# Performance work log

Hardware: AMD Instinct MI355X
Metric: run time of the kernel (lower is better)

Reference implementation:

```python
import jax, jax.numpy as jnp
import numpy as np

N_NODES = 100000


def _gcn_layer(h, W, b, src, dst, norm, n):
    # h: [N, Fin] -> transform then normalized scatter-add aggregation
    h = h @ W                                   # [N, Fout]
    msg = h[src] * norm[:, None]                # [E', Fout] gather + scale
    out = jax.ops.segment_sum(msg, dst, num_segments=n)  # scatter-add
    return out + b


def setup_inputs() -> dict:
    key = jax.random.key(0)
    k1, k2, k3, k4 = jax.random.split(key, 4)
    N, F_IN, HID, C, E = N_NODES, 512, 128, 40, 1600000
    x = jax.random.normal(k1, (N, F_IN), dtype=jnp.float32)
    edge_index = jax.random.randint(k2, (2, E), 0, N, dtype=jnp.int64)
    W1 = jax.random.normal(k3, (F_IN, HID), dtype=jnp.float32) * (1.0 / np.sqrt(F_IN))
    b1 = jnp.zeros((HID,), dtype=jnp.float32)
    W2 = jax.random.normal(k4, (HID, C), dtype=jnp.float32) * (1.0 / np.sqrt(HID))
    b2 = jnp.zeros((C,), dtype=jnp.float32)
    return {"x": x, "edge_index": edge_index, "W1": W1, "b1": b1, "W2": W2, "b2": b2}


def reference(x, edge_index, W1, b1, W2, b2):
    n = x.shape[0]
    # add self-loops (GCNConv default)
    loop = jnp.arange(n, dtype=edge_index.dtype)
    src = jnp.concatenate([edge_index[0], loop])
    dst = jnp.concatenate([edge_index[1], loop])
    # symmetric normalization: deg counted on destination (in-degree, incl. self-loop)
    deg = jax.ops.segment_sum(jnp.ones_like(dst, dtype=x.dtype), dst, num_segments=n)
    dis = jnp.where(deg > 0, jax.lax.rsqrt(deg), 0.0)  # deg^{-1/2}
    norm = dis[src] * dis[dst]                          # per-edge weight

    h = jax.nn.relu(_gcn_layer(x, W1, b1, src, dst, norm, n))
    # dropout: identity in eval mode (training=False)
    h = _gcn_layer(h, W2, b2, src, dst, norm, n)
    return jax.nn.log_softmax(h, axis=1)
```

## Files before the change

kernel.cpp:

```cpp
#include <hip/hip_runtime.h>
#include <hip/hip_bf16.h>


#define F_IN 512
#define HID  128
#define NC   40

typedef __attribute__((ext_vector_type(8))) short bf16x8;
typedef __attribute__((ext_vector_type(4))) float f32x4v;

__device__ __forceinline__ ushort f2bf(float f) {
    union { float f; unsigned u; } x; x.f = f;
    unsigned r = x.u + 0x7FFFu + ((x.u >> 16) & 1u);
    return (ushort)(r >> 16);
}
__device__ __forceinline__ float bf2f(ushort u) {
    return __uint_as_float((unsigned)u << 16);
}

__global__ void count_deg(const int* __restrict__ dst, int E, unsigned* __restrict__ cnt) {
    int t = blockIdx.x * blockDim.x + threadIdx.x;
    if (t < E) atomicAdd(&cnt[dst[t]], 1u);
}

__global__ __launch_bounds__(1024) void scan_block(const unsigned* __restrict__ cnt,
                                                   unsigned* __restrict__ offs,
                                                   unsigned* __restrict__ bsums,
                                                   float* __restrict__ dis, int N) {
    __shared__ unsigned s[1024];
    int tid = threadIdx.x;
    int i = blockIdx.x * 1024 + tid;
    unsigned v = (i < N) ? cnt[i] : 0u;
    if (i < N) dis[i] = rsqrtf((float)v + 1.0f);
    s[tid] = v;
    __syncthreads();
    #pragma unroll
    for (int d = 1; d < 1024; d <<= 1) {
        unsigned t = (tid >= d) ? s[tid - d] : 0u;
        __syncthreads();
        s[tid] += t;
        __syncthreads();
    }
    if (i < N) offs[i] = s[tid] - v;
    if (tid == 1023) bsums[blockIdx.x] = s[1023];
}

__global__ __launch_bounds__(1024) void scan_bsums(unsigned* __restrict__ bsums, int nb) {
    __shared__ unsigned s[1024];
    int tid = threadIdx.x;
    unsigned v = (tid < nb) ? bsums[tid] : 0u;
    s[tid] = v;
    __syncthreads();
    #pragma unroll
    for (int d = 1; d < 1024; d <<= 1) {
        unsigned t = (tid >= d) ? s[tid - d] : 0u;
        __syncthreads();
        s[tid] += t;
        __syncthreads();
    }
    if (tid < nb) bsums[tid] = s[tid] - v;
}

__global__ __launch_bounds__(1024) void scan_add(unsigned* __restrict__ offs,
                                                 const unsigned* __restrict__ bsums,
                                                 int N, unsigned total) {
    int i = blockIdx.x * 1024 + threadIdx.x;
    if (i < N) offs[i] += bsums[blockIdx.x];
    if (i == 0) offs[N] = total;
}

__global__ void fill_csr(const int* __restrict__ src, const int* __restrict__ dst,
                         const unsigned* __restrict__ offs, unsigned* __restrict__ cursor,
                         int* __restrict__ col, int E) {
    int t = blockIdx.x * blockDim.x + threadIdx.x;
    if (t >= E) return;
    int s = src[t], d = dst[t];
    unsigned pos = offs[d] + atomicAdd(&cursor[d], 1u);
    col[pos] = s;
}

__global__ void packW(const float* __restrict__ W1, const float* __restrict__ W2,
                      ushort* __restrict__ W1p, ushort* __restrict__ W2p) {
    int t = blockIdx.x * 256 + threadIdx.x;
    if (t < 65536) {
        int j = t & 7, n = (t >> 3) & 127, kb = (t >> 10) & 3, s = t >> 12;
        int k = s * 32 + kb * 8 + j;
        W1p[t] = f2bf(W1[(size_t)k * HID + n]);
    } else {
        int q = t - 65536;
        if (q < 6144) {
            int j = q & 7;
            int i2 = q >> 3;
            int n = i2 % 48;
            int i3 = i2 / 48;
            int kb = i3 & 3, ks = i3 >> 2;
            int k = ks * 32 + kb * 8 + j;
            float v = (n < NC) ? W2[(size_t)k * NC + n] : 0.f;
            W2p[q] = f2bf(v);
        }
    }
}

__global__ __launch_bounds__(256) void gemm1_mfma(const float* __restrict__ A,
                                                  const ushort* __restrict__ Bp,
                                                  const float* __restrict__ dis,
                                                  ushort* __restrict__ C, int N) {
    __shared__ __align__(16) ushort Bs[2][4096];
    const int tid  = threadIdx.x;
    const int wave = tid >> 6;
    const int lane = tid & 63;
    const int quad = lane >> 4;
    const int mr   = lane & 15;
    const int bm   = blockIdx.x * 64;
    const int row  = bm + wave * 16 + mr;
    const bool ok  = row < N;
    const float* aptr = A + (size_t)(ok ? row : 0) * F_IN + quad * 8;

    f32x4v acc[8];
    #pragma unroll
    for (int t = 0; t < 8; t++) acc[t] = (f32x4v){0.f, 0.f, 0.f, 0.f};

    const float4 z4 = make_float4(0.f, 0.f, 0.f, 0.f);
    float4 av[2][2];
    uint4 bv0, bv1;

    av[0][0] = ok ? *(const float4*)(aptr)      : z4;
    av[0][1] = ok ? *(const float4*)(aptr + 4)  : z4;
    av[1][0] = ok ? *(const float4*)(aptr + 32) : z4;
    av[1][1] = ok ? *(const float4*)(aptr + 36) : z4;
    ((uint4*)Bs[0])[tid]       = ((const uint4*)Bp)[tid];
    ((uint4*)Bs[0])[tid + 256] = ((const uint4*)Bp)[tid + 256];
    {
        const uint4* bp = (const uint4*)(Bp + 4096);
        bv0 = bp[tid];
        bv1 = bp[tid + 256];
    }
    __syncthreads();

    for (int s = 0; s < 16; s++) {
        float4 a0 = av[s & 1][0], a1 = av[s & 1][1];
        __align__(16) ushort ta[8];
        ta[0]=f2bf(a0.x); ta[1]=f2bf(a0.y); ta[2]=f2bf(a0.z); ta[3]=f2bf(a0.w);
        ta[4]=f2bf(a1.x); ta[5]=f2bf(a1.y); ta[6]=f2bf(a1.z); ta[7]=f2bf(a1.w);
        bf16x8 fa = *(const bf16x8*)ta;
        if (s < 15) {
            ((uint4*)Bs[(s + 1) & 1])[tid]       = bv0;
            ((uint4*)Bs[(s + 1) & 1])[tid + 256] = bv1;
        }
        if (s < 14) {
            const uint4* bp = (const uint4*)(Bp + (size_t)(s + 2) * 4096);
            bv0 = bp[tid];
            bv1 = bp[tid + 256];
        }
        if (s + 2 < 16) {
            av[s & 1][0] = ok ? *(const float4*)(aptr + (s + 2) * 32)     : z4;
            av[s & 1][1] = ok ? *(const float4*)(aptr + (s + 2) * 32 + 4) : z4;
        }
        {
            const ushort* bb = Bs[s & 1] + quad * 1024 + mr * 8;
            #pragma unroll
            for (int t = 0; t < 8; t++) {
                bf16x8 b = *(const bf16x8*)&bb[t * 128];
                acc[t] = __builtin_amdgcn_mfma_f32_16x16x32_bf16(fa, b, acc[t], 0, 0, 0);
            }
        }
        __syncthreads();
    }

    #pragma unroll
    for (int rr = 0; rr < 4; rr++) {
        int r = bm + wave * 16 + quad * 4 + rr;
        if (r < N) {
            float ds = dis[r];
            #pragma unroll
            for (int t = 0; t < 8; t++)
                C[(size_t)r * HID + t * 16 + mr] = f2bf(acc[t][rr] * ds);
        }
    }
}

__global__ __launch_bounds__(256) void agg1_k(const ushort* __restrict__ h,
                                              const int* __restrict__ col,
                                              const unsigned* __restrict__ offs,
                                              const float* __restrict__ dis,
                                              ushort* __restrict__ out, int N) {
    int node = blockIdx.x * 16 + (threadIdx.x >> 4);
    if (node >= N) return;
    int lane = threadIdx.x & 15;
    const size_t coff = (size_t)lane * 8;
    float a[8];
    {
        uint4 v = *(const uint4*)(h + (size_t)node * HID + coff);
        const ushort* u = (const ushort*)&v;
        #pragma unroll
        for (int j = 0; j < 8; j++) a[j] = bf2f(u[j]);
    }
    unsigned p0 = offs[node], p1 = offs[node + 1];
    unsigned p = p0;
    for (; p + 8 <= p1; p += 8) {
        int s0 = col[p],   s1 = col[p+1], s2 = col[p+2], s3 = col[p+3];
        int s4 = col[p+4], s5 = col[p+5], s6 = col[p+6], s7 = col[p+7];
        uint4 v0 = *(const uint4*)(h + (size_t)s0 * HID + coff);
        uint4 v1 = *(const uint4*)(h + (size_t)s1 * HID + coff);
        uint4 v2 = *(const uint4*)(h + (size_t)s2 * HID + coff);
        uint4 v3 = *(const uint4*)(h + (size_t)s3 * HID + coff);
        uint4 v4 = *(const uint4*)(h + (size_t)s4 * HID + coff);
        uint4 v5 = *(const uint4*)(h + (size_t)s5 * HID + coff);
        uint4 v6 = *(const uint4*)(h + (size_t)s6 * HID + coff);
        uint4 v7 = *(const uint4*)(h + (size_t)s7 * HID + coff);
        const ushort* u0 = (const ushort*)&v0;
        const ushort* u1 = (const ushort*)&v1;
        const ushort* u2 = (const ushort*)&v2;
        const ushort* u3 = (const ushort*)&v3;
        const ushort* u4 = (const ushort*)&v4;
        const ushort* u5 = (const ushort*)&v5;
        const ushort* u6 = (const ushort*)&v6;
        const ushort* u7 = (const ushort*)&v7;
        #pragma unroll
        for (int j = 0; j < 8; j++) {
            float t0 = bf2f(u0[j]) + bf2f(u1[j]);
            float t1 = bf2f(u2[j]) + bf2f(u3[j]);
            float t2 = bf2f(u4[j]) + bf2f(u5[j]);
            float t3 = bf2f(u6[j]) + bf2f(u7[j]);
            a[j] += (t0 + t1) + (t2 + t3);
        }
    }
    for (; p < p1; ++p) {
        int s = col[p];
        uint4 v = *(const uint4*)(h + (size_t)s * HID + coff);
        const ushort* u = (const ushort*)&v;
        #pragma unroll
        for (int j = 0; j < 8; j++) a[j] += bf2f(u[j]);
    }
    float dd = dis[node];
    __align__(16) ushort o[8];
    #pragma unroll
    for (int j = 0; j < 8; j++) o[j] = f2bf(a[j] * dd);
    *(uint4*)(out + (size_t)node * HID + coff) = *(const uint4*)o;
}

__global__ __launch_bounds__(256) void gemm2_mfma(const ushort* __restrict__ A,
                                                  const float* __restrict__ b1,
                                                  const ushort* __restrict__ W2p,
                                                  const float* __restrict__ dis,
                                                  ushort* __restrict__ h2, int N) {
    __shared__ __align__(16) ushort As[128 * 136];
    __shared__ __align__(16) ushort Bs[6144];
    const int tid = threadIdx.x;
    const int bm = blockIdx.x * 128;

    {
        const uint4* s4 = (const uint4*)W2p;
        uint4* d4 = (uint4*)Bs;
        #pragma unroll
        for (int i = 0; i < 3; i++) d4[tid + i * 256] = s4[tid + i * 256];
    }
    {
        const int r  = tid >> 1;
        const int hh = tid & 1;
        const int row = bm + r;
        const float* brow = b1 + hh * 64;
        if (row < N) {
            const ushort* arow = A + (size_t)row * HID + hh * 64;
            #pragma unroll
            for (int i = 0; i < 8; i++) {
                uint4 raw = *(const uint4*)(arow + i * 8);
                const ushort* u = (const ushort*)&raw;
                __align__(16) ushort tmp[8];
                #pragma unroll
                for (int j = 0; j < 8; j++)
                    tmp[j] = f2bf(fmaxf(bf2f(u[j]) + brow[i * 8 + j], 0.f));
                *(uint4*)&As[r * 136 + hh * 64 + i * 8] = *(const uint4*)tmp;
            }
        } else {
            #pragma unroll
            for (int i = 0; i < 8; i++) {
                uint4 zz = {0, 0, 0, 0};
                *(uint4*)&As[r * 136 + hh * 64 + i * 8] = zz;
            }
        }
    }
    __syncthreads();

    const int wave = tid >> 6;
    const int lane = tid & 63;
    const int quad = lane >> 4;
    const int mr   = lane & 15;
    f32x4v acc[2][3];
    #pragma unroll
    for (int i = 0; i < 2; i++)
        #pragma unroll
        for (int t = 0; t < 3; t++)
            acc[i][t] = (f32x4v){0.f, 0.f, 0.f, 0.f};
    #pragma unroll
    for (int ks = 0; ks < 4; ks++) {
        bf16x8 a0 = *(const bf16x8*)&As[(wave * 32 + mr) * 136 + ks * 32 + quad * 8];
        bf16x8 a1 = *(const bf16x8*)&As[(wave * 32 + 16 + mr) * 136 + ks * 32 + quad * 8];
        #pragma unroll
        for (int t = 0; t < 3; t++) {
            bf16x8 b = *(const bf16x8*)&Bs[((ks * 4 + quad) * 48 + t * 16 + mr) * 8];
            acc[0][t] = __builtin_amdgcn_mfma_f32_16x16x32_bf16(a0, b, acc[0][t], 0, 0, 0);
            acc[1][t] = __builtin_amdgcn_mfma_f32_16x16x32_bf16(a1, b, acc[1][t], 0, 0, 0);
        }
    }
    #pragma unroll
    for (int i = 0; i < 2; i++) {
        #pragma unroll
        for (int rr = 0; rr < 4; rr++) {
            int node = bm + wave * 32 + i * 16 + quad * 4 + rr;
            if (node < N) {
                float ds = dis[node];
                #pragma unroll
                for (int t = 0; t < 3; t++) {
                    int c = t * 16 + mr;
                    if (c < NC)
                        h2[(size_t)node * NC + c] = f2bf(acc[i][t][rr] * ds);
                }
            }
        }
    }
}

__global__ __launch_bounds__(256) void agg2_ls(const ushort* __restrict__ h2,
                                               const int* __restrict__ col,
                                               const unsigned* __restrict__ offs,
                                               const float* __restrict__ dis,
                                               const float* __restrict__ b2,
                                               float* __restrict__ out, int N) {
    int node = blockIdx.x * 32 + (threadIdx.x >> 3);
    if (node >= N) return;
    int lane = threadIdx.x & 7;
    const bool act = lane < 5;
    const size_t coff = (size_t)lane * 8;
    float a[8] = {};
    if (act) {
        uint4 v = *(const uint4*)(h2 + (size_t)node * NC + coff);
        const ushort* u = (const ushort*)&v;
        #pragma unroll
        for (int j = 0; j < 8; j++) a[j] = bf2f(u[j]);
    }
    unsigned p0 = offs[node], p1 = offs[node + 1];
    unsigned p = p0;
    for (; p + 4 <= p1; p += 4) {
        int s0 = col[p], s1 = col[p + 1], s2 = col[p + 2], s3 = col[p + 3];
        if (act) {
            uint4 v0 = *(const uint4*)(h2 + (size_t)s0 * NC + coff);
            uint4 v1 = *(const uint4*)(h2 + (size_t)s1 * NC + coff);
            uint4 v2 = *(const uint4*)(h2 + (size_t)s2 * NC + coff);
            uint4 v3 = *(const uint4*)(h2 + (size_t)s3 * NC + coff);
            const ushort* u0 = (const ushort*)&v0;
            const ushort* u1 = (const ushort*)&v1;
            const ushort* u2 = (const ushort*)&v2;
            const ushort* u3 = (const ushort*)&v3;
            #pragma unroll
            for (int j = 0; j < 8; j++)
                a[j] += (bf2f(u0[j]) + bf2f(u1[j])) + (bf2f(u2[j]) + bf2f(u3[j]));
        }
    }
    for (; p < p1; ++p) {
        int s = col[p];
        if (act) {
            uint4 v = *(const uint4*)(h2 + (size_t)s * NC + coff);
            const ushort* u = (const ushort*)&v;
            #pragma unroll
            for (int j = 0; j < 8; j++) a[j] += bf2f(u[j]);
        }
    }
    float dd = dis[node];
    float l[8];
    float m = -1e30f;
    if (act) {
        #pragma unroll
        for (int j = 0; j < 8; j++) {
            l[j] = a[j] * dd + b2[lane * 8 + j];
            m = fmaxf(m, l[j]);
        }
    }
    #pragma unroll
    for (int d = 1; d < 8; d <<= 1) m = fmaxf(m, __shfl_xor(m, d, 8));
    float s = 0.f;
    if (act) {
        #pragma unroll
        for (int j = 0; j < 8; j++) s += __expf(l[j] - m);
    }
    #pragma unroll
    for (int d = 1; d < 8; d <<= 1) s += __shfl_xor(s, d, 8);
    float lse = m + __logf(s);
    if (act) {
        float* op = out + (size_t)node * NC + lane * 8;
        *(float4*)op       = make_float4(l[0]-lse, l[1]-lse, l[2]-lse, l[3]-lse);
        *(float4*)(op + 4) = make_float4(l[4]-lse, l[5]-lse, l[6]-lse, l[7]-lse);
    }
}

extern "C" void kernel_launch(void* const* d_in, const int* in_sizes, int n_in,
                              void* d_out, int out_size, void* d_ws, size_t ws_size,
                              hipStream_t stream) {
    const float* x  = (const float*)d_in[0];
    const int*   ei = (const int*)d_in[1];
    const float* W1 = (const float*)d_in[2];
    const float* b1 = (const float*)d_in[3];
    const float* W2 = (const float*)d_in[4];
    const float* b2 = (const float*)d_in[5];
    float* out = (float*)d_out;

    const int N = in_sizes[0] / F_IN;
    const int E = in_sizes[1] / 2;
    const int* src = ei;
    const int* dst = ei + E;

    char* ws = (char*)d_ws;
    size_t o = 0;
    unsigned* cnt  = (unsigned*)(ws + o); o += (size_t)N * 4;
    unsigned* cur  = (unsigned*)(ws + o); o += (size_t)N * 4;
    float*    dis  = (float*)   (ws + o); o += (size_t)N * 4;
    unsigned* offs = (unsigned*)(ws + o); o += (size_t)(N + 4) * 4;
    unsigned* bsums= (unsigned*)(ws + o); o += 4096;
    int*      col  = (int*)     (ws + o); o += (size_t)E * 4;
    o = (o + 15) & ~(size_t)15;
    ushort*   W1p  = (ushort*)  (ws + o); o += (size_t)F_IN * HID * 2;
    o = (o + 15) & ~(size_t)15;
    ushort*   W2p  = (ushort*)  (ws + o); o += 6144 * 2;
    o = (o + 15) & ~(size_t)15;
    ushort*   h1   = (ushort*)  (ws + o); o += (size_t)N * HID * 2;
    o = (o + 15) & ~(size_t)15;
    ushort*   ag1  = (ushort*)  (ws + o); o += (size_t)N * HID * 2;
    o = (o + 15) & ~(size_t)15;
    ushort*   h2   = (ushort*)  (ws + o); o += (size_t)N * NC * 2;

    const int nb = (N + 1023) / 1024;

    hipMemsetAsync(cnt, 0, (size_t)N * 8, stream);
    count_deg<<<(E + 255) / 256, 256, 0, stream>>>(dst, E, cnt);
    scan_block<<<nb, 1024, 0, stream>>>(cnt, offs, bsums, dis, N);
    scan_bsums<<<1, 1024, 0, stream>>>(bsums, nb);
    scan_add<<<nb, 1024, 0, stream>>>(offs, bsums, N, (unsigned)E);
    fill_csr<<<(E + 255) / 256, 256, 0, stream>>>(src, dst, offs, cur, col, E);

    packW<<<(65536 + 6144 + 255) / 256, 256, 0, stream>>>(W1, W2, W1p, W2p);

    gemm1_mfma<<<(N + 63) / 64, 256, 0, stream>>>(x, W1p, dis, h1, N);
    agg1_k<<<(N + 15) / 16, 256, 0, stream>>>(h1, col, offs, dis, ag1, N);

    gemm2_mfma<<<(N + 127) / 128, 256, 0, stream>>>(ag1, b1, W2p, dis, h2, N);
    agg2_ls<<<(N + 31) / 32, 256, 0, stream>>>(h2, col, offs, dis, b2, out, N);
}
```

Before: 647.8 us.

## Drop LDS staging in GEMMs, double rows per wave, fuse bias+ReLU into aggregation

gemm1 now has each wave compute 32 rows with two accumulator sets and read packed W1 fragments straight from global/L2. This removes the double-buffered shared memory and the per-step block barriers. gemm2 likewise reads A and W2 directly from global memory, without the LDS tile. The bias add and ReLU move from gemm2's prologue into agg1's epilogue, which also avoids rounding to bf16 twice. The risk is more redundant global/L2 traffic for B, since every wave reloads the full weight, and higher register pressure from 16 accumulators.

After: 616.8 us. 1.05x faster.

```diff
diff --git a/kernel.cpp b/kernel.cpp
--- a/kernel.cpp
+++ b/kernel.cpp
@@ -16,6 +16,12 @@
 }
 __device__ __forceinline__ float bf2f(ushort u) {
     return __uint_as_float((unsigned)u << 16);
+}
+__device__ __forceinline__ bf16x8 cvt8(float4 lo, float4 hi) {
+    __align__(16) ushort t[8];
+    t[0]=f2bf(lo.x); t[1]=f2bf(lo.y); t[2]=f2bf(lo.z); t[3]=f2bf(lo.w);
+    t[4]=f2bf(hi.x); t[5]=f2bf(hi.y); t[6]=f2bf(hi.z); t[7]=f2bf(hi.w);
+    return *(const bf16x8*)t;
 }
 
 __global__ void count_deg(const int* __restrict__ dst, int E, unsigned* __restrict__ cnt) {
@@ -105,76 +111,69 @@
                                                   const ushort* __restrict__ Bp,
                                                   const float* __restrict__ dis,
                                                   ushort* __restrict__ C, int N) {
-    __shared__ __align__(16) ushort Bs[2][4096];
     const int tid  = threadIdx.x;
     const int wave = tid >> 6;
     const int lane = tid & 63;
     const int quad = lane >> 4;
     const int mr   = lane & 15;
-    const int bm   = blockIdx.x * 64;
-    const int row  = bm + wave * 16 + mr;
-    const bool ok  = row < N;
-    const float* aptr = A + (size_t)(ok ? row : 0) * F_IN + quad * 8;
-
-    f32x4v acc[8];
-    #pragma unroll
-    for (int t = 0; t < 8; t++) acc[t] = (f32x4v){0.f, 0.f, 0.f, 0.f};
-
-    const float4 z4 = make_float4(0.f, 0.f, 0.f, 0.f);
-    float4 av[2][2];
-    uint4 bv0, bv1;
-
-    av[0][0] = ok ? *(const float4*)(aptr)      : z4;
-    av[0][1] = ok ? *(const float4*)(aptr + 4)  : z4;
-    av[1][0] = ok ? *(const float4*)(aptr + 32) : z4;
-    av[1][1] = ok ? *(const float4*)(aptr + 36) : z4;
-    ((uint4*)Bs[0])[tid]       = ((const uint4*)Bp)[tid];
-    ((uint4*)Bs[0])[tid + 256] = ((const uint4*)Bp)[tid + 256];
-    {
-        const uint4* bp = (const uint4*)(Bp + 4096);
-        bv0 = bp[tid];
-        bv1 = bp[tid + 256];
-    }
-    __syncthreads();
+    const int base = (blockIdx.x * 4 + wave) * 32;
+    if (base >= N) return;
+    const int r0 = base + mr;
+    const int r1 = base + 16 + mr;
+    const bool ok0 = r0 < N, ok1 = r1 < N;
+    const float* ap0 = A + (size_t)(ok0 ? r0 : 0) * F_IN + quad * 8;
+    const float* ap1 = A + (size_t)(ok1 ? r1 : 0) * F_IN + quad * 8;
+    const ushort* bp = Bp + quad * 1024 + mr * 8;
+
+    f32x4v acc0[8], acc1[8];
+    #pragma unroll
+    for (int t = 0; t < 8; t++) {
+        acc0[t] = (f32x4v){0.f, 0.f, 0.f, 0.f};
+        acc1[t] = (f32x4v){0.f, 0.f, 0.f, 0.f};
+    }
+
+    float4 av[2][4];
+    #pragma unroll
+    for (int b = 0; b < 2; b++) {
+        av[b][0] = *(const float4*)(ap0 + b * 32);
+        av[b][1] = *(const float4*)(ap0 + b * 32 + 4);
+        av[b][2] = *(const float4*)(ap1 + b * 32);
+        av[b][3] = *(const float4*)(ap1 + b * 32 + 4);
+    }
 
     for (int s = 0; s < 16; s++) {
-        float4 a0 = av[s & 1][0], a1 = av[s & 1][1];
-        __align__(16) ushort ta[8];
-        ta[0]=f2bf(a0.x); ta[1]=f2bf(a0.y); ta[2]=f2bf(a0.z); ta[3]=f2bf(a0.w);
-        ta[4]=f2bf(a1.x); ta[5]=f2bf(a1.y); ta[6]=f2bf(a1.z); ta[7]=f2bf(a1.w);
-        bf16x8 fa = *(const bf16x8*)ta;
-        if (s < 15) {
-            ((uint4*)Bs[(s + 1) & 1])[tid]       = bv0;
-            ((uint4*)Bs[(s + 1) & 1])[tid + 256] = bv1;
-        }
+        bf16x8 fa0 = cvt8(av[s & 1][0], av[s & 1][1]);
+        bf16x8 fa1 = cvt8(av[s & 1][2], av[s & 1][3]);
         if (s < 14) {
-            const uint4* bp = (const uint4*)(Bp + (size_t)(s + 2) * 4096);
-            bv0 = bp[tid];
-            bv1 = bp[tid + 256];
-        }
-        if (s + 2 < 16) {
-            av[s & 1][0] = ok ? *(const float4*)(aptr + (s + 2) * 32)     : z4;
-            av[s & 1][1] = ok ? *(const float4*)(aptr + (s + 2) * 32 + 4) : z4;
-        }
-        {
-            const ushort* bb = Bs[s & 1] + quad * 1024 + mr * 8;
-            #pragma unroll
-            for (int t = 0; t < 8; t++) {
-                bf16x8 b = *(const bf16x8*)&bb[t * 128];
-                acc[t] = __builtin_amdgcn_mfma_f32_16x16x32_bf16(fa, b, acc[t], 0, 0, 0);
-            }
-        }
-        __syncthreads();
+            av[s & 1][0] = *(const float4*)(ap0 + (s + 2) * 32);
+            av[s & 1][1] = *(const float4*)(ap0 + (s + 2) * 32 + 4);
+            av[s & 1][2] = *(const float4*)(ap1 + (s + 2) * 32);
+            av[s & 1][3] = *(const float4*)(ap1 + (s + 2) * 32 + 4);
+        }
+        const ushort* bs = bp + s * 4096;
+        #pragma unroll
+        for (int t = 0; t < 8; t++) {
+            bf16x8 b = *(const bf16x8*)(bs + t * 128);
+            acc0[t] = __builtin_amdgcn_mfma_f32_16x16x32_bf16(fa0, b, acc0[t], 0, 0, 0);
+            acc1[t] = __builtin_amdgcn_mfma_f32_16x16x32_bf16(fa1, b, acc1[t], 0, 0, 0);
+        }
     }
 
     #pragma unroll
     for (int rr = 0; rr < 4; rr++) {
-        int r = bm + wave * 16 + quad * 4 + rr;
-        if (r < N) {
-            float ds = dis[r];
+        int ra = base + quad * 4 + rr;
+        if (ra < N) {
+            float ds = dis[ra];
             #pragma unroll
             for (int t = 0; t < 8; t++)
-                C[(size_t)r * HID + t * 16 + mr] = f2bf(acc[t][rr] * ds);
+                C[(size_t)ra * HID + t * 16 + mr] = f2bf(acc0[t][rr] * ds);
+        }
+        int rb = base + 16 + quad * 4 + rr;
+        if (rb < N) {
+            float ds = dis[rb];
+            #pragma unroll
+            for (int t = 0; t < 8; t++)
+                C[(size_t)rb * HID + t * 16 + mr] = f2bf(acc1[t][rr] * ds);
         }
     }
 }
@@ -183,6 +182,7 @@
                                               const int* __restrict__ col,
                                               const unsigned* __restrict__ offs,
                                               const float* __restrict__ dis,
+                                              const float* __restrict__ b1,
                                               ushort* __restrict__ out, int N) {
     int node = blockIdx.x * 16 + (threadIdx.x >> 4);
     if (node >= N) return;
@@ -233,89 +233,68 @@
         for (int j = 0; j < 8; j++) a[j] += bf2f(u[j]);
     }
     float dd = dis[node];
+    float4 bb0 = *(const float4*)(b1 + lane * 8);
+    float4 bb1 = *(const float4*)(b1 + lane * 8 + 4);
+    const float bb[8] = {bb0.x, bb0.y, bb0.z, bb0.w, bb1.x, bb1.y, bb1.z, bb1.w};
     __align__(16) ushort o[8];
     #pragma unroll
-    for (int j = 0; j < 8; j++) o[j] = f2bf(a[j] * dd);
+    for (int j = 0; j < 8; j++) o[j] = f2bf(fmaxf(a[j] * dd + bb[j], 0.f));
     *(uint4*)(out + (size_t)node * HID + coff) = *(const uint4*)o;
 }
 
 __global__ __launch_bounds__(256) void gemm2_mfma(const ushort* __restrict__ A,
-                                                  const float* __restrict__ b1,
                                                   const ushort* __restrict__ W2p,
                                                   const float* __restrict__ dis,
                                                   ushort* __restrict__ h2, int N) {
-    __shared__ __align__(16) ushort As[128 * 136];
-    __shared__ __align__(16) ushort Bs[6144];
-    const int tid = threadIdx.x;
-    const int bm = blockIdx.x * 128;
-
-    {
-        const uint4* s4 = (const uint4*)W2p;
-        uint4* d4 = (uint4*)Bs;
-        #pragma unroll
-        for (int i = 0; i < 3; i++) d4[tid + i * 256] = s4[tid + i * 256];
-    }
-    {
-        const int r  = tid >> 1;
-        const int hh = tid & 1;
-        const int row = bm + r;
-        const float* brow = b1 + hh * 64;
-        if (row < N) {
-            const ushort* arow = A + (size_t)row * HID + hh * 64;
-            #pragma unroll
-            for (int i = 0; i < 8; i++) {
-                uint4 raw = *(const uint4*)(arow + i * 8);
-                const ushort* u = (const ushort*)&raw;
-                __align__(16) ushort tmp[8];
-                #pragma unroll
-                for (int j = 0; j < 8; j++)
-                    tmp[j] = f2bf(fmaxf(bf2f(u[j]) + brow[i * 8 + j], 0.f));
-                *(uint4*)&As[r * 136 + hh * 64 + i * 8] = *(const uint4*)tmp;
-            }
-        } else {
-            #pragma unroll
-            for (int i = 0; i < 8; i++) {
-                uint4 zz = {0, 0, 0, 0};
-                *(uint4*)&As[r * 136 + hh * 64 + i * 8] = zz;
-            }
-        }
-    }
-    __syncthreads();
-
+    const int tid  = threadIdx.x;
     const int wave = tid >> 6;
     const int lane = tid & 63;
     const int quad = lane >> 4;
     const int mr   = lane & 15;
-    f32x4v acc[2][3];
-    #pragma unroll
-    for (int i = 0; i < 2; i++)
-        #pragma unroll
-        for (int t = 0; t < 3; t++)
-            acc[i][t] = (f32x4v){0.f, 0.f, 0.f, 0.f};
+    const int base = (blockIdx.x * 4 + wave) * 32;
+    if (base >= N) return;
+    const int r0 = base + mr;
+    const int r1 = base + 16 + mr;
+    const bool ok0 = r0 < N, ok1 = r1 < N;
+    const ushort* ap0 = A + (size_t)(ok0 ? r0 : 0) * HID + quad * 8;
+    const ushort* ap1 = A + (size_t)(ok1 ? r1 : 0) * HID + quad * 8;
+    const ushort* bp = W2p + quad * 384 + mr * 8;
+
+    f32x4v acc0[3], acc1[3];
+    #pragma unroll
+    for (int t = 0; t < 3; t++) {
+        acc0[t] = (f32x4v){0.f, 0.f, 0.f, 0.f};
+        acc1[t] = (f32x4v){0.f, 0.f, 0.f, 0.f};
+    }
     #pragma unroll
     for (int ks = 0; ks < 4; ks++) {
-        bf16x8 a0 = *(const bf16x8*)&As[(wave * 32 + mr) * 136 + ks * 32 + quad * 8];
-        bf16x8 a1 = *(const bf16x8*)&As[(wave * 32 + 16 + mr) * 136 + ks * 32 + quad * 8];
+        bf16x8 a0 = *(const bf16x8*)(ap0 + ks * 32);
+        bf16x8 a1 = *(const bf16x8*)(ap1 + ks * 32);
         #pragma unroll
         for (int t = 0; t < 3; t++) {
-            bf16x8 b = *(const bf16x8*)&Bs[((ks * 4 + quad) * 48 + t * 16 + mr) * 8];
-            acc[0][t] = __builtin_amdgcn_mfma_f32_16x16x32_bf16(a0, b, acc[0][t], 0, 0, 0);
-            acc[1][t] = __builtin_amdgcn_mfma_f32_16x16x32_bf16(a1, b, acc[1][t], 0, 0, 0);
-        }
-    }
-    #pragma unroll
-    for (int i = 0; i < 2; i++) {
-        #pragma unroll
-        for (int rr = 0; rr < 4; rr++) {
-            int node = bm + wave * 32 + i * 16 + quad * 4 + rr;
-            if (node < N) {
-                float ds = dis[node];
-                #pragma unroll
-                for (int t = 0; t < 3; t++) {
-                    int c = t * 16 + mr;
-                    if (c < NC)
-                        h2[(size_t)node * NC + c] = f2bf(acc[i][t][rr] * ds);
-                }
+            bf16x8 b = *(const bf16x8*)(bp + ks * 1536 + t * 128);
+            acc0[t] = __builtin_amdgcn_mfma_f32_16x16x32_bf16(a0, b, acc0[t], 0, 0, 0);
+            acc1[t] = __builtin_amdgcn_mfma_f32_16x16x32_bf16(a1, b, acc1[t], 0, 0, 0);
+        }
+    }
+    #pragma unroll
+    for (int rr = 0; rr < 4; rr++) {
+        int ra = base + quad * 4 + rr;
+        if (ra < N) {
+            float ds = dis[ra];
+            #pragma unroll
+            for (int t = 0; t < 3; t++) {
+                int c = t * 16 + mr;
+                if (c < NC) h2[(size_t)ra * NC + c] = f2bf(acc0[t][rr] * ds);
+            }
+        }
+        int rb = base + 16 + quad * 4 + rr;
+        if (rb < N) {
+            float ds = dis[rb];
+            #pragma unroll
+            for (int t = 0; t < 3; t++) {
+                int c = t * 16 + mr;
+                if (c < NC) h2[(size_t)rb * NC + c] = f2bf(acc1[t][rr] * ds);
             }
         }
     }
@@ -439,9 +418,9 @@
 
     packW<<<(65536 + 6144 + 255) / 256, 256, 0, stream>>>(W1, W2, W1p, W2p);
 
-    gemm1_mfma<<<(N + 63) / 64, 256, 0, stream>>>(x, W1p, dis, h1, N);
-    agg1_k<<<(N + 15) / 16, 256, 0, stream>>>(h1, col, offs, dis, ag1, N);
-
-    gemm2_mfma<<<(N + 127) / 128, 256, 0, stream>>>(ag1, b1, W2p, dis, h2, N);
+    gemm1_mfma<<<(N + 127) / 128, 256, 0, stream>>>(x, W1p, dis, h1, N);
+    agg1_k<<<(N + 15) / 16, 256, 0, stream>>>(h1, col, offs, dis, b1, ag1, N);
+
+    gemm2_mfma<<<(N + 127) / 128, 256, 0, stream>>>(ag1, W2p, dis, h2, N);
     agg2_ls<<<(N + 31) / 32, 256, 0, stream>>>(h2, col, offs, dis, b2, out, N);
 }
```
